# Performance work log

Hardware: AMD Instinct MI355X
Metric: run time of the kernel (lower is better)

The kernel has to match this reference:

```python
import jax, jax.numpy as jnp
import numpy as np

CURV_BOUNDS = (-2.0, 2.0)
THRESH = 0.01   # |k| below this -> Euclidean branch
EPS = 1e-5

B, S, D = 4, 2048, 512


def setup_inputs() -> dict:
    key = jax.random.key(0)
    ks = jax.random.split(key, 8)
    x = jax.random.normal(ks[0], (B, S, D), jnp.float32)
    sc = 1.0 / np.sqrt(D)  # ~ nn.Linear default init scale
    Wq = jax.random.uniform(ks[1], (D, D), jnp.float32, -sc, sc)
    bq = jax.random.uniform(ks[2], (D,), jnp.float32, -sc, sc)
    Wk = jax.random.uniform(ks[3], (D, D), jnp.float32, -sc, sc)
    bk = jax.random.uniform(ks[4], (D,), jnp.float32, -sc, sc)
    Wv = jax.random.uniform(ks[5], (D, D), jnp.float32, -sc, sc)
    bv = jax.random.uniform(ks[6], (D,), jnp.float32, -sc, sc)
    curvature_raw = jnp.float32(0.5)   # init_curvature
    temperature = jnp.float32(1.0)
    mask = jnp.triu(jnp.ones((S, S), dtype=bool), 1)  # causal: True = masked out
    return {"x": x, "Wq": Wq, "bq": bq, "Wk": Wk, "bk": bk, "Wv": Wv,
            "bv": bv, "curvature_raw": curvature_raw,
            "temperature": temperature, "mask": mask}


def _curvature(raw):
    k_min, k_max = CURV_BOUNDS
    return k_min + (k_max - k_min) * (jnp.tanh(raw) + 1.0) / 2.0


def _project(u, k):
    # project_to_manifold: identity (euclid), Poincare-ball clip (k<0), sphere renorm (k>0)
    n = jnp.sqrt(jnp.sum(u * u, axis=-1, keepdims=True) + 1e-12)
    absk = jnp.abs(k)
    sk = jnp.sqrt(jnp.maximum(absk, EPS))
    max_norm = (1.0 - 1e-3) / sk                      # ball radius 1/sqrt(|k|)
    u_hyp = u * jnp.minimum(1.0, max_norm / n)
    u_sph = u / (n * sk)                              # sphere radius 1/sqrt(k)
    return jnp.where(absk < THRESH, u, jnp.where(k < 0, u_hyp, u_sph))


def reference(x, Wq, bq, Wk, bk, Wv, bv, curvature_raw, temperature, mask):
    k = _curvature(curvature_raw)
    q = x @ Wq.T + bq
    kk = x @ Wk.T + bk
    v = x @ Wv.T + bv
    qm = _project(q, k)
    km = _project(kk, k)

    # pairwise quantities without materializing [B,S,S,D]
    dots = jnp.einsum('bid,bjd->bij', qm, km)         # [B,S,S]
    qn2 = jnp.sum(qm * qm, axis=-1)                   # [B,S]
    kn2 = jnp.sum(km * km, axis=-1)                   # [B,S]
    diff2 = jnp.maximum(qn2[:, :, None] + kn2[:, None, :] - 2.0 * dots, 0.0)

    absk = jnp.abs(k)
    sk = jnp.sqrt(jnp.maximum(absk, EPS))

    d_euc = jnp.sqrt(diff2 + 1e-12)
    # hyperbolic (Poincare ball, c=|k|): acosh(1 + 2c|x-y|^2 / ((1-c|x|^2)(1-c|y|^2))) / sqrt(c)
    denom = jnp.maximum((1.0 - absk * qn2)[:, :, None] * (1.0 - absk * kn2)[:, None, :], EPS)
    arg = 1.0 + 2.0 * absk * diff2 / denom
    d_hyp = jnp.arccosh(jnp.maximum(arg, 1.0 + 1e-7)) / sk
    # spherical (radius 1/sqrt(k)): arccos(k * <x,y>) / sqrt(k)
    cosang = jnp.clip(absk * dots, -1.0 + 1e-7, 1.0 - 1e-7)
    d_sph = jnp.arccos(cosang) / sk

    dist = jnp.where(absk < THRESH, d_euc, jnp.where(k < 0, d_hyp, d_sph))

    scores = -dist / (temperature + 1e-8)
    scores = jnp.where(mask[None, :, :], -jnp.inf, scores)
    attention = jax.nn.softmax(scores, axis=-1)       # [B,S,S]
    output = jnp.einsum('bij,bjd->bid', attention, v) # [B,S,D]
    return output, attention
```

## Files before the change

### kernel.cpp

```cpp
#include <hip/hip_runtime.h>
#include <hip/hip_bf16.h>
#include <math.h>

typedef unsigned short u16;
typedef float float4e __attribute__((ext_vector_type(4)));
typedef short short8 __attribute__((ext_vector_type(8)));

#define SEQ 2048
#define DIM 512
#define NB  4

__device__ __forceinline__ float bf2f(u16 h) {
    return __uint_as_float(((unsigned)h) << 16);
}
__device__ __forceinline__ u16 f2bf(float f) {
    __hip_bfloat16 h = __float2bfloat16(f);
    return *reinterpret_cast<u16*>(&h);
}
__device__ __forceinline__ float curv_of(float raw) {
    return -2.0f + 2.0f * (tanhf(raw) + 1.0f);
}
__device__ __forceinline__ void gl_lds16(const u16* g, u16* lds) {
    __builtin_amdgcn_global_load_lds(
        (const __attribute__((address_space(1))) unsigned int*)g,
        (__attribute__((address_space(3))) unsigned int*)lds, 16, 0, 0);
}

__global__ __launch_bounds__(256) void cvt_all_kernel(
    const float* __restrict__ x, const float* __restrict__ Wq,
    const float* __restrict__ Wk, const float* __restrict__ Wv,
    u16* __restrict__ x_bf, u16* __restrict__ Wcat, float* __restrict__ lsum)
{
    int i = blockIdx.x * 256 + threadIdx.x;
    const int n_x = NB * SEQ * DIM, n_w = DIM * DIM;
    if (i < NB * SEQ) lsum[i] = 0.f;
    if (i < n_x) {
        x_bf[i] = f2bf(x[i]);
    } else if (i < n_x + 3 * n_w) {
        int j = i - n_x;
        const float* W = (j < n_w) ? Wq : (j < 2 * n_w ? Wk : Wv);
        int off = j % n_w;
        Wcat[j] = f2bf(W[off]);
    }
}

__global__ __launch_bounds__(256) void qkv_gemm_kernel(
    const u16* __restrict__ A,
    const u16* __restrict__ Bt,
    u16* __restrict__ C,
    const float* __restrict__ bq, const float* __restrict__ bk, const float* __restrict__ bv)
{
    int bn = blockIdx.x, bm = blockIdx.y;
    __shared__ __align__(16) u16 As[128 * 32];
    __shared__ __align__(16) u16 Bs[128 * 32];

    int t = threadIdx.x, wave = t >> 6, lane = t & 63;
    int wm = wave >> 1, wn = wave & 1;
    int lrow = lane & 15, quad = lane >> 4;
    int lr4 = lane >> 2, lch = lane & 3;

    float4e acc[4][4];
#pragma unroll
    for (int i = 0; i < 4; i++)
#pragma unroll
        for (int j = 0; j < 4; j++) acc[i][j] = (float4e){0.f, 0.f, 0.f, 0.f};

    for (int kt = 0; kt < 16; ++kt) {
        int k0 = kt << 5;
        __syncthreads();
#pragma unroll
        for (int h = 0; h < 2; ++h) {
            int q = wave + h * 4;
            int row = q * 16 + lr4;
            gl_lds16(A  + (size_t)(bm * 128 + row) * 512 + k0 + lch * 8, &As[q * 512]);
            gl_lds16(Bt + (size_t)(bn * 128 + row) * 512 + k0 + lch * 8, &Bs[q * 512]);
        }
        __syncthreads();

        short8 af[4], bfr[4];
#pragma unroll
        for (int im = 0; im < 4; im++)
            af[im] = *(const short8*)&As[(wm * 64 + im * 16 + lrow) * 32 + quad * 8];
#pragma unroll
        for (int in = 0; in < 4; in++)
            bfr[in] = *(const short8*)&Bs[(wn * 64 + in * 16 + lrow) * 32 + quad * 8];
#pragma unroll
        for (int im = 0; im < 4; im++)
#pragma unroll
            for (int in = 0; in < 4; in++)
                acc[im][in] = __builtin_amdgcn_mfma_f32_16x16x32_bf16(af[im], bfr[in], acc[im][in], 0, 0, 0);
    }

#pragma unroll
    for (int im = 0; im < 4; im++)
#pragma unroll
        for (int in = 0; in < 4; in++)
#pragma unroll
            for (int r = 0; r < 4; r++) {
                int i = bm * 128 + wm * 64 + im * 16 + quad * 4 + r;
                int j = bn * 128 + wn * 64 + in * 16 + lrow;
                float bias = (j < 512) ? bq[j] : (j < 1024 ? bk[j - 512] : bv[j - 1024]);
                C[(size_t)i * 1536 + j] = f2bf(acc[im][in][r] + bias);
            }
}

__global__ __launch_bounds__(256) void project_kernel(
    const u16* __restrict__ qkvh,
    u16* __restrict__ qm, u16* __restrict__ km,
    float* __restrict__ qn2, float* __restrict__ kn2,
    const float* __restrict__ curvp)
{
    int r = blockIdx.x;
    int t = threadIdx.x;
    float kv = curv_of(curvp[0]);
    float absk = fabsf(kv);
    float sk = sqrtf(fmaxf(absk, 1e-5f));

    const u16* qrow = qkvh + (size_t)r * 1536;
    const u16* krow = qrow + 512;
    float q0 = bf2f(qrow[t]), q1 = bf2f(qrow[t + 256]);
    float k0 = bf2f(krow[t]), k1 = bf2f(krow[t + 256]);

    float sq = q0 * q0 + q1 * q1;
    float s2 = k0 * k0 + k1 * k1;
#pragma unroll
    for (int off = 32; off > 0; off >>= 1) {
        sq += __shfl_down(sq, off);
        s2 += __shfl_down(s2, off);
    }
    __shared__ float rq[4], rk[4];
    int wave = t >> 6, lane = t & 63;
    if (lane == 0) { rq[wave] = sq; rk[wave] = s2; }
    __syncthreads();
    float n2q = rq[0] + rq[1] + rq[2] + rq[3];
    float n2k = rk[0] + rk[1] + rk[2] + rk[3];

    float sclq, sclk;
    {
        float nq = sqrtf(n2q + 1e-12f);
        float nk = sqrtf(n2k + 1e-12f);
        if (absk < 0.01f) { sclq = 1.f; sclk = 1.f; }
        else if (kv < 0.f) {
            float mx = (1.0f - 1e-3f) / sk;
            sclq = fminf(1.f, mx / nq);
            sclk = fminf(1.f, mx / nk);
        } else {
            sclq = 1.f / (nq * sk);
            sclk = 1.f / (nk * sk);
        }
    }
    if (t == 0) {
        qn2[r] = n2q * sclq * sclq;
        kn2[r] = n2k * sclk * sclk;
    }
    u16* qo = qm + (size_t)r * 512;
    u16* ko = km + (size_t)r * 512;
    qo[t]       = f2bf(q0 * sclq);
    qo[t + 256] = f2bf(q1 * sclq);
    ko[t]       = f2bf(k0 * sclk);
    ko[t + 256] = f2bf(k1 * sclk);
}

__global__ __launch_bounds__(256) void transpose_v_kernel(
    const u16* __restrict__ qkvh, u16* __restrict__ vT)
{
    __shared__ u16 tile[32][33];
    int b = blockIdx.z;
    int s0 = blockIdx.x * 32, d0 = blockIdx.y * 32;
    int tx = threadIdx.x, ty = threadIdx.y;
#pragma unroll
    for (int r = 0; r < 4; r++) {
        int s = s0 + ty + r * 8;
        tile[ty + r * 8][tx] = qkvh[(size_t)(b * SEQ + s) * 1536 + 1024 + d0 + tx];
    }
    __syncthreads();
#pragma unroll
    for (int r = 0; r < 4; r++) {
        int d = d0 + ty + r * 8;
        int s = s0 + tx;
        vT[((size_t)b * DIM + d) * SEQ + s] = tile[tx][ty + r * 8];
    }
}

__global__ __launch_bounds__(256) void scores_kernel(
    const u16* __restrict__ qm, const u16* __restrict__ km,
    const float* __restrict__ qn2v, const float* __restrict__ kn2v,
    float* __restrict__ attnF, u16* __restrict__ attnH, float* __restrict__ lsum,
    const float* __restrict__ curvp, const float* __restrict__ tempp)
{
    int bn = blockIdx.x, bm = blockIdx.y, b = blockIdx.z;
    if (bn > bm) return;

    __shared__ __align__(16) u16 As[64 * 32];
    __shared__ __align__(16) u16 Bs[64 * 32];

    int t = threadIdx.x, wave = t >> 6, lane = t & 63;
    int wr = wave >> 1, wc = wave & 1;
    int lrow = lane & 15, quad = lane >> 4;
    int lr4 = lane >> 2, lch = lane & 3;

    const u16* Ab = qm + (size_t)b * SEQ * DIM;
    const u16* Bb = km + (size_t)b * SEQ * DIM;

    float4e acc[2][2];
#pragma unroll
    for (int i = 0; i < 2; i++)
#pragma unroll
        for (int j = 0; j < 2; j++) acc[i][j] = (float4e){0.f, 0.f, 0.f, 0.f};

    for (int kt = 0; kt < 16; ++kt) {
        int k0 = kt << 5;
        __syncthreads();
        int row = wave * 16 + lr4;
        gl_lds16(Ab + (size_t)(bm * 64 + row) * 512 + k0 + lch * 8, &As[wave * 512]);
        gl_lds16(Bb + (size_t)(bn * 64 + row) * 512 + k0 + lch * 8, &Bs[wave * 512]);
        __syncthreads();

        short8 af[2], bfr[2];
#pragma unroll
        for (int im = 0; im < 2; im++)
            af[im] = *(const short8*)&As[(wr * 32 + im * 16 + lrow) * 32 + quad * 8];
#pragma unroll
        for (int in = 0; in < 2; in++)
            bfr[in] = *(const short8*)&Bs[(wc * 32 + in * 16 + lrow) * 32 + quad * 8];
#pragma unroll
        for (int im = 0; im < 2; im++)
#pragma unroll
            for (int in = 0; in < 2; in++)
                acc[im][in] = __builtin_amdgcn_mfma_f32_16x16x32_bf16(af[im], bfr[in], acc[im][in], 0, 0, 0);
    }

    float kv = curv_of(curvp[0]);
    float absk = fabsf(kv);
    float sk = sqrtf(fmaxf(absk, 1e-5f));
    float invT = 1.0f / (tempp[0] + 1e-8f);

    float* attF = attnF + (size_t)b * SEQ * SEQ;
    u16*   attH = attnH + (size_t)b * SEQ * SEQ;

    float psum[2][4];
#pragma unroll
    for (int im = 0; im < 2; im++)
#pragma unroll
        for (int r = 0; r < 4; r++) psum[im][r] = 0.f;

#pragma unroll
    for (int im = 0; im < 2; im++) {
#pragma unroll
        for (int r = 0; r < 4; r++) {
            int gi = bm * 64 + wr * 32 + im * 16 + quad * 4 + r;
            float qn = qn2v[b * SEQ + gi];
#pragma unroll
            for (int in = 0; in < 2; in++) {
                int gj = bn * 64 + wc * 32 + in * 16 + lrow;
                float kn = kn2v[b * SEQ + gj];
                float dot = acc[im][in][r];
                float diff2 = fmaxf(qn + kn - 2.f * dot, 0.f);
                float dist;
                if (absk < 0.01f) {
                    dist = sqrtf(diff2 + 1e-12f);
                } else if (kv < 0.f) {
                    float denom = fmaxf((1.f - absk * qn) * (1.f - absk * kn), 1e-5f);
                    float arg = fmaxf(1.f + 2.f * absk * diff2 / denom, 1.f + 1e-7f);
                    dist = acoshf(arg) / sk;
                } else {
                    float c = fminf(fmaxf(absk * dot, -1.f + 1e-7f), 1.f - 1e-7f);
                    dist = acosf(c) / sk;
                }
                float s = -dist * invT;
                float e = (gj <= gi) ? __expf(s) : 0.f;
                attF[(size_t)gi * SEQ + gj] = e;
                attH[(size_t)gi * SEQ + gj] = f2bf(e);
                psum[im][r] += e;
            }
        }
    }

#pragma unroll
    for (int im = 0; im < 2; im++)
#pragma unroll
        for (int r = 0; r < 4; r++) {
            float v = psum[im][r];
            v += __shfl_xor(v, 1);
            v += __shfl_xor(v, 2);
            v += __shfl_xor(v, 4);
            v += __shfl_xor(v, 8);
            if (lrow == 0) {
                int gi = bm * 64 + wr * 32 + im * 16 + quad * 4 + r;
                atomicAdd(&lsum[b * SEQ + gi], v);
            }
        }
}

__global__ __launch_bounds__(256) void pv_kernel(
    const u16* __restrict__ attnH,
    const u16* __restrict__ vT,
    const float* __restrict__ lsum,
    float* __restrict__ out)
{
    int bn = blockIdx.x, bm = blockIdx.y, b = blockIdx.z;

    __shared__ __align__(16) u16 As[64 * 32];
    __shared__ __align__(16) u16 Bs[64 * 32];

    int t = threadIdx.x, wave = t >> 6, lane = t & 63;
    int wr = wave >> 1, wc = wave & 1;
    int lrow = lane & 15, quad = lane >> 4;
    int lr4 = lane >> 2, lch = lane & 3;

    const u16* Ab = attnH + (size_t)b * SEQ * SEQ;
    const u16* Bb = vT + (size_t)b * DIM * SEQ;

    float4e acc[2][2];
#pragma unroll
    for (int i = 0; i < 2; i++)
#pragma unroll
        for (int j = 0; j < 2; j++) acc[i][j] = (float4e){0.f, 0.f, 0.f, 0.f};

    int kIters = (bm + 1) * 2;
    for (int kt = 0; kt < kIters; ++kt) {
        int k0 = kt << 5;
        __syncthreads();
        int row = wave * 16 + lr4;
        gl_lds16(Ab + (size_t)(bm * 64 + row) * SEQ + k0 + lch * 8, &As[wave * 512]);
        gl_lds16(Bb + (size_t)(bn * 64 + row) * SEQ + k0 + lch * 8, &Bs[wave * 512]);
        __syncthreads();

        short8 af[2], bfr[2];
#pragma unroll
        for (int im = 0; im < 2; im++)
            af[im] = *(const short8*)&As[(wr * 32 + im * 16 + lrow) * 32 + quad * 8];
#pragma unroll
        for (int in = 0; in < 2; in++)
            bfr[in] = *(const short8*)&Bs[(wc * 32 + in * 16 + lrow) * 32 + quad * 8];
#pragma unroll
        for (int im = 0; im < 2; im++)
#pragma unroll
            for (int in = 0; in < 2; in++)
                acc[im][in] = __builtin_amdgcn_mfma_f32_16x16x32_bf16(af[im], bfr[in], acc[im][in], 0, 0, 0);
    }

#pragma unroll
    for (int im = 0; im < 2; im++)
#pragma unroll
        for (int r = 0; r < 4; r++) {
            int gi = bm * 64 + wr * 32 + im * 16 + quad * 4 + r;
            float invl = 1.0f / lsum[b * SEQ + gi];
#pragma unroll
            for (int in = 0; in < 2; in++) {
                int gd = bn * 64 + wc * 32 + in * 16 + lrow;
                out[((size_t)b * SEQ + gi) * DIM + gd] = acc[im][in][r] * invl;
            }
        }
}

__global__ __launch_bounds__(256) void norm_attn_kernel(
    float* __restrict__ attnF, const float* __restrict__ lsum)
{
    int i = blockIdx.x, b = blockIdx.y, t = threadIdx.x;
    float inv = 1.0f / lsum[b * SEQ + i];
    float4* row = (float4*)(attnF + ((size_t)b * SEQ + i) * SEQ);
#pragma unroll
    for (int c = t; c < SEQ / 4; c += 256) {
        int j0 = c * 4;
        float4 v = row[c];
        v.x = (j0     <= i) ? v.x * inv : 0.f;
        v.y = (j0 + 1 <= i) ? v.y * inv : 0.f;
        v.z = (j0 + 2 <= i) ? v.z * inv : 0.f;
        v.w = (j0 + 3 <= i) ? v.w * inv : 0.f;
        row[c] = v;
    }
}

extern "C" void kernel_launch(void* const* d_in, const int* in_sizes, int n_in,
                              void* d_out, int out_size, void* d_ws, size_t ws_size,
                              hipStream_t stream) {
    (void)in_sizes; (void)n_in; (void)out_size; (void)ws_size;

    const float* x    = (const float*)d_in[0];
    const float* Wq   = (const float*)d_in[1];
    const float* bq   = (const float*)d_in[2];
    const float* Wk   = (const float*)d_in[3];
    const float* bk   = (const float*)d_in[4];
    const float* Wv   = (const float*)d_in[5];
    const float* bv   = (const float*)d_in[6];
    const float* curv = (const float*)d_in[7];
    const float* temp = (const float*)d_in[8];

    float* out   = (float*)d_out;
    float* attnF = out + (size_t)NB * SEQ * DIM;

    char* ws = (char*)d_ws;
    u16*   x_bf  = (u16*)(ws + 0);
    u16*   Wcat  = (u16*)(ws + 8388608);
    u16*   qkvh  = (u16*)(ws + 9961472);
    u16*   qm    = (u16*)(ws + 35127296);
    u16*   km    = (u16*)(ws + 43515904);
    u16*   vT    = (u16*)(ws + 51904512);
    float* qn2   = (float*)(ws + 60293120);
    float* kn2   = (float*)(ws + 60325888);
    float* lsum  = (float*)(ws + 60358656);
    u16*   attnH = (u16*)(ws + 0);

    {
        int n_tot = NB * SEQ * DIM + 3 * DIM * DIM;
        cvt_all_kernel<<<(n_tot + 255) / 256, 256, 0, stream>>>(x, Wq, Wk, Wv, x_bf, Wcat, lsum);
    }

    {
        dim3 g(1536 / 128, 8192 / 128, 1);
        qkv_gemm_kernel<<<g, 256, 0, stream>>>(x_bf, Wcat, qkvh, bq, bk, bv);
    }

    project_kernel<<<NB * SEQ, 256, 0, stream>>>(qkvh, qm, km, qn2, kn2, curv);

    {
        dim3 g(SEQ / 32, DIM / 32, NB), blk(32, 8);
        transpose_v_kernel<<<g, blk, 0, stream>>>(qkvh, vT);
    }

    {
        dim3 g(SEQ / 64, SEQ / 64, NB);
        scores_kernel<<<g, 256, 0, stream>>>(qm, km, qn2, kn2, attnF, attnH, lsum, curv, temp);
    }

    {
        dim3 g(DIM / 64, SEQ / 64, NB);
        pv_kernel<<<g, 256, 0, stream>>>(attnH, vT, lsum, out);
    }

    norm_attn_kernel<<<dim3(SEQ, NB), 256, 0, stream>>>(attnF, lsum);
}
```

Baseline: 265.9 us.

## Unify GEMMs into templated 64x64 kernel with deeper K tiles and swizzled LDS

```diff
diff --git a/kernel.cpp b/kernel.cpp
--- a/kernel.cpp
+++ b/kernel.cpp
@@ -5,6 +5,7 @@
 typedef unsigned short u16;
 typedef float float4e __attribute__((ext_vector_type(4)));
 typedef short short8 __attribute__((ext_vector_type(8)));
+typedef unsigned short ushort8 __attribute__((ext_vector_type(8)));
 
 #define SEQ 2048
 #define DIM 512
@@ -44,64 +45,167 @@
     }
 }
 
-__global__ __launch_bounds__(256) void qkv_gemm_kernel(
-    const u16* __restrict__ A,
-    const u16* __restrict__ Bt,
-    u16* __restrict__ C,
-    const float* __restrict__ bq, const float* __restrict__ bk, const float* __restrict__ bv)
-{
-    int bn = blockIdx.x, bm = blockIdx.y;
-    __shared__ __align__(16) u16 As[128 * 32];
-    __shared__ __align__(16) u16 Bs[128 * 32];
-
+template<int MODE>
+__global__ __launch_bounds__(256) void gemm64_kernel(
+    const u16* __restrict__ A, int lda, long long sA,
+    const u16* __restrict__ Bt, int ldb, long long sB,
+    void* __restrict__ Cv, int ldc, long long sC,
+    float* __restrict__ lsum,
+    const float* __restrict__ bq, const float* __restrict__ bk, const float* __restrict__ bv,
+    const float* __restrict__ qn2v, const float* __restrict__ kn2v,
+    const float* __restrict__ curvp, const float* __restrict__ tempp)
+{
+    int bn = blockIdx.x, bm = blockIdx.y, b = blockIdx.z;
     int t = threadIdx.x, wave = t >> 6, lane = t & 63;
-    int wm = wave >> 1, wn = wave & 1;
+
+    if (MODE == 1) {
+        if (bn > bm) {
+            if (bn == bm + 1 && !(bm & 1)) {
+                u16* Cb = (u16*)Cv + (size_t)b * sC;
+                int r = t >> 2, seg = t & 3;
+                int4 z = {0, 0, 0, 0};
+                int4* p = (int4*)&Cb[(size_t)(bm * 64 + r) * ldc + bn * 64 + seg * 16];
+                p[0] = z; p[1] = z;
+            }
+            return;
+        }
+    }
+
+    __shared__ __align__(16) u16 As[64 * 128];
+    __shared__ __align__(16) u16 Bs[64 * 128];
+
+    int wr = wave >> 1, wc = wave & 1;
     int lrow = lane & 15, quad = lane >> 4;
-    int lr4 = lane >> 2, lch = lane & 3;
-
-    float4e acc[4][4];
-#pragma unroll
-    for (int i = 0; i < 4; i++)
-#pragma unroll
-        for (int j = 0; j < 4; j++) acc[i][j] = (float4e){0.f, 0.f, 0.f, 0.f};
-
-    for (int kt = 0; kt < 16; ++kt) {
-        int k0 = kt << 5;
+    int rl = lane >> 4, cs = lane & 15;
+
+    const u16* Ab = A + (size_t)b * sA + (size_t)(bm * 64) * lda;
+    const u16* Bb = Bt + (size_t)b * sB + (size_t)(bn * 64) * ldb;
+
+    float4e acc[2][2];
+#pragma unroll
+    for (int i = 0; i < 2; i++)
+#pragma unroll
+        for (int j = 0; j < 2; j++) acc[i][j] = (float4e){0.f, 0.f, 0.f, 0.f};
+
+    int kIters = (MODE == 2) ? ((bm + 2) >> 1) : 4;
+
+    for (int kt = 0; kt < kIters; ++kt) {
+        int k0 = kt << 7;
         __syncthreads();
 #pragma unroll
-        for (int h = 0; h < 2; ++h) {
-            int q = wave + h * 4;
-            int row = q * 16 + lr4;
-            gl_lds16(A  + (size_t)(bm * 128 + row) * 512 + k0 + lch * 8, &As[q * 512]);
-            gl_lds16(Bt + (size_t)(bn * 128 + row) * 512 + k0 + lch * 8, &Bs[q * 512]);
+        for (int h = 0; h < 4; ++h) {
+            int row = wave * 16 + h * 4 + rl;
+            int c = cs ^ (row & 15);
+            gl_lds16(Ab + (size_t)row * lda + k0 + c * 8, &As[(wave * 16 + h * 4) * 128]);
+            gl_lds16(Bb + (size_t)row * ldb + k0 + c * 8, &Bs[(wave * 16 + h * 4) * 128]);
         }
         __syncthreads();
-
-        short8 af[4], bfr[4];
-#pragma unroll
-        for (int im = 0; im < 4; im++)
-            af[im] = *(const short8*)&As[(wm * 64 + im * 16 + lrow) * 32 + quad * 8];
-#pragma unroll
-        for (int in = 0; in < 4; in++)
-            bfr[in] = *(const short8*)&Bs[(wn * 64 + in * 16 + lrow) * 32 + quad * 8];
-#pragma unroll
-        for (int im = 0; im < 4; im++)
-#pragma unroll
-            for (int in = 0; in < 4; in++)
-                acc[im][in] = __builtin_amdgcn_mfma_f32_16x16x32_bf16(af[im], bfr[in], acc[im][in], 0, 0, 0);
-    }
-
-#pragma unroll
-    for (int im = 0; im < 4; im++)
-#pragma unroll
-        for (int in = 0; in < 4; in++)
+#pragma unroll
+        for (int s = 0; s < 4; ++s) {
+            short8 af[2], bfr[2];
+#pragma unroll
+            for (int im = 0; im < 2; im++) {
+                int row = wr * 32 + im * 16 + lrow;
+                af[im] = *(const short8*)&As[(row * 16 + ((s * 4 + quad) ^ (row & 15))) * 8];
+            }
+#pragma unroll
+            for (int in = 0; in < 2; in++) {
+                int row = wc * 32 + in * 16 + lrow;
+                bfr[in] = *(const short8*)&Bs[(row * 16 + ((s * 4 + quad) ^ (row & 15))) * 8];
+            }
+#pragma unroll
+            for (int im = 0; im < 2; im++)
+#pragma unroll
+                for (int in = 0; in < 2; in++)
+                    acc[im][in] = __builtin_amdgcn_mfma_f32_16x16x32_bf16(af[im], bfr[in], acc[im][in], 0, 0, 0);
+        }
+    }
+
+    if (MODE == 0) {
+        u16* Cb = (u16*)Cv;
+#pragma unroll
+        for (int im = 0; im < 2; im++)
+#pragma unroll
+            for (int in = 0; in < 2; in++)
+#pragma unroll
+                for (int r = 0; r < 4; r++) {
+                    int gi = bm * 64 + wr * 32 + im * 16 + quad * 4 + r;
+                    int gj = bn * 64 + wc * 32 + in * 16 + lrow;
+                    float bias = (gj < 512) ? bq[gj] : (gj < 1024 ? bk[gj - 512] : bv[gj - 1024]);
+                    Cb[(size_t)gi * ldc + gj] = f2bf(acc[im][in][r] + bias);
+                }
+    } else if (MODE == 1) {
+        float kv = curv_of(curvp[0]);
+        float absk = fabsf(kv);
+        float sk = sqrtf(fmaxf(absk, 1e-5f));
+        float invT = 1.0f / (tempp[0] + 1e-8f);
+        u16* Cb = (u16*)Cv + (size_t)b * sC;
+
+        float psum[2][4];
+#pragma unroll
+        for (int im = 0; im < 2; im++)
+#pragma unroll
+            for (int r = 0; r < 4; r++) psum[im][r] = 0.f;
+
+#pragma unroll
+        for (int im = 0; im < 2; im++) {
 #pragma unroll
             for (int r = 0; r < 4; r++) {
-                int i = bm * 128 + wm * 64 + im * 16 + quad * 4 + r;
-                int j = bn * 128 + wn * 64 + in * 16 + lrow;
-                float bias = (j < 512) ? bq[j] : (j < 1024 ? bk[j - 512] : bv[j - 1024]);
-                C[(size_t)i * 1536 + j] = f2bf(acc[im][in][r] + bias);
-            }
+                int gi = bm * 64 + wr * 32 + im * 16 + quad * 4 + r;
+                float qn = qn2v[b * SEQ + gi];
+#pragma unroll
+                for (int in = 0; in < 2; in++) {
+                    int gj = bn * 64 + wc * 32 + in * 16 + lrow;
+                    float kn = kn2v[b * SEQ + gj];
+                    float dot = acc[im][in][r];
+                    float diff2 = fmaxf(qn + kn - 2.f * dot, 0.f);
+                    float dist;
+                    if (absk < 0.01f) {
+                        dist = sqrtf(diff2 + 1e-12f);
+                    } else if (kv < 0.f) {
+                        float denom = fmaxf((1.f - absk * qn) * (1.f - absk * kn), 1e-5f);
+                        float arg = fmaxf(1.f + 2.f * absk * diff2 / denom, 1.f + 1e-7f);
+                        dist = acoshf(arg) / sk;
+                    } else {
+                        float c = fminf(fmaxf(absk * dot, -1.f + 1e-7f), 1.f - 1e-7f);
+                        dist = acosf(c) / sk;
+                    }
+                    float s = -dist * invT;
+                    float e = (gj <= gi) ? __expf(s) : 0.f;
+                    Cb[(size_t)gi * ldc + gj] = f2bf(e);
+                    psum[im][r] += e;
+                }
+            }
+        }
+#pragma unroll
+        for (int im = 0; im < 2; im++)
+#pragma unroll
+            for (int r = 0; r < 4; r++) {
+                float v = psum[im][r];
+                v += __shfl_xor(v, 1);
+                v += __shfl_xor(v, 2);
+                v += __shfl_xor(v, 4);
+                v += __shfl_xor(v, 8);
+                if (lrow == 0) {
+                    int gi = bm * 64 + wr * 32 + im * 16 + quad * 4 + r;
+                    atomicAdd(&lsum[b * SEQ + gi], v);
+                }
+            }
+    } else {
+        float* Cb = (float*)Cv + (size_t)b * sC;
+#pragma unroll
+        for (int im = 0; im < 2; im++)
+#pragma unroll
+            for (int r = 0; r < 4; r++) {
+                int gi = bm * 64 + wr * 32 + im * 16 + quad * 4 + r;
+                float invl = 1.0f / lsum[b * SEQ + gi];
+#pragma unroll
+                for (int in = 0; in < 2; in++) {
+                    int gd = bn * 64 + wc * 32 + in * 16 + lrow;
+                    Cb[(size_t)gi * ldc + gd] = acc[im][in][r] * invl;
+                }
+            }
+    }
 }
 
 __global__ __launch_bounds__(256) void project_kernel(
@@ -182,194 +286,33 @@
     }
 }
 
-__global__ __launch_bounds__(256) void scores_kernel(
-    const u16* __restrict__ qm, const u16* __restrict__ km,
-    const float* __restrict__ qn2v, const float* __restrict__ kn2v,
-    float* __restrict__ attnF, u16* __restrict__ attnH, float* __restrict__ lsum,
-    const float* __restrict__ curvp, const float* __restrict__ tempp)
-{
-    int bn = blockIdx.x, bm = blockIdx.y, b = blockIdx.z;
-    if (bn > bm) return;
-
-    __shared__ __align__(16) u16 As[64 * 32];
-    __shared__ __align__(16) u16 Bs[64 * 32];
-
-    int t = threadIdx.x, wave = t >> 6, lane = t & 63;
-    int wr = wave >> 1, wc = wave & 1;
-    int lrow = lane & 15, quad = lane >> 4;
-    int lr4 = lane >> 2, lch = lane & 3;
-
-    const u16* Ab = qm + (size_t)b * SEQ * DIM;
-    const u16* Bb = km + (size_t)b * SEQ * DIM;
-
-    float4e acc[2][2];
-#pragma unroll
-    for (int i = 0; i < 2; i++)
-#pragma unroll
-        for (int j = 0; j < 2; j++) acc[i][j] = (float4e){0.f, 0.f, 0.f, 0.f};
-
-    for (int kt = 0; kt < 16; ++kt) {
-        int k0 = kt << 5;
-        __syncthreads();
-        int row = wave * 16 + lr4;
-        gl_lds16(Ab + (size_t)(bm * 64 + row) * 512 + k0 + lch * 8, &As[wave * 512]);
-        gl_lds16(Bb + (size_t)(bn * 64 + row) * 512 + k0 + lch * 8, &Bs[wave * 512]);
-        __syncthreads();
-
-        short8 af[2], bfr[2];
-#pragma unroll
-        for (int im = 0; im < 2; im++)
-            af[im] = *(const short8*)&As[(wr * 32 + im * 16 + lrow) * 32 + quad * 8];
-#pragma unroll
-        for (int in = 0; in < 2; in++)
-            bfr[in] = *(const short8*)&Bs[(wc * 32 + in * 16 + lrow) * 32 + quad * 8];
-#pragma unroll
-        for (int im = 0; im < 2; im++)
-#pragma unroll
-            for (int in = 0; in < 2; in++)
-                acc[im][in] = __builtin_amdgcn_mfma_f32_16x16x32_bf16(af[im], bfr[in], acc[im][in], 0, 0, 0);
-    }
-
-    float kv = curv_of(curvp[0]);
-    float absk = fabsf(kv);
-    float sk = sqrtf(fmaxf(absk, 1e-5f));
-    float invT = 1.0f / (tempp[0] + 1e-8f);
-
-    float* attF = attnF + (size_t)b * SEQ * SEQ;
-    u16*   attH = attnH + (size_t)b * SEQ * SEQ;
-
-    float psum[2][4];
-#pragma unroll
-    for (int im = 0; im < 2; im++)
-#pragma unroll
-        for (int r = 0; r < 4; r++) psum[im][r] = 0.f;
-
-#pragma unroll
-    for (int im = 0; im < 2; im++) {
-#pragma unroll
-        for (int r = 0; r < 4; r++) {
-            int gi = bm * 64 + wr * 32 + im * 16 + quad * 4 + r;
-            float qn = qn2v[b * SEQ + gi];
-#pragma unroll
-            for (int in = 0; in < 2; in++) {
-                int gj = bn * 64 + wc * 32 + in * 16 + lrow;
-                float kn = kn2v[b * SEQ + gj];
-                float dot = acc[im][in][r];
-                float diff2 = fmaxf(qn + kn - 2.f * dot, 0.f);
-                float dist;
-                if (absk < 0.01f) {
-                    dist = sqrtf(diff2 + 1e-12f);
-                } else if (kv < 0.f) {
-                    float denom = fmaxf((1.f - absk * qn) * (1.f - absk * kn), 1e-5f);
-                    float arg = fmaxf(1.f + 2.f * absk * diff2 / denom, 1.f + 1e-7f);
-                    dist = acoshf(arg) / sk;
-                } else {
-                    float c = fminf(fmaxf(absk * dot, -1.f + 1e-7f), 1.f - 1e-7f);
-                    dist = acosf(c) / sk;
-                }
-                float s = -dist * invT;
-                float e = (gj <= gi) ? __expf(s) : 0.f;
-                attF[(size_t)gi * SEQ + gj] = e;
-                attH[(size_t)gi * SEQ + gj] = f2bf(e);
-                psum[im][r] += e;
-            }
-        }
-    }
-
-#pragma unroll
-    for (int im = 0; im < 2; im++)
-#pragma unroll
-        for (int r = 0; r < 4; r++) {
-            float v = psum[im][r];
-            v += __shfl_xor(v, 1);
-            v += __shfl_xor(v, 2);
-            v += __shfl_xor(v, 4);
-            v += __shfl_xor(v, 8);
-            if (lrow == 0) {
-                int gi = bm * 64 + wr * 32 + im * 16 + quad * 4 + r;
-                atomicAdd(&lsum[b * SEQ + gi], v);
-            }
-        }
-}
-
-__global__ __launch_bounds__(256) void pv_kernel(
-    const u16* __restrict__ attnH,
-    const u16* __restrict__ vT,
-    const float* __restrict__ lsum,
-    float* __restrict__ out)
-{
-    int bn = blockIdx.x, bm = blockIdx.y, b = blockIdx.z;
-
-    __shared__ __align__(16) u16 As[64 * 32];
-    __shared__ __align__(16) u16 Bs[64 * 32];
-
-    int t = threadIdx.x, wave = t >> 6, lane = t & 63;
-    int wr = wave >> 1, wc = wave & 1;
-    int lrow = lane & 15, quad = lane >> 4;
-    int lr4 = lane >> 2, lch = lane & 3;
-
-    const u16* Ab = attnH + (size_t)b * SEQ * SEQ;
-    const u16* Bb = vT + (size_t)b * DIM * SEQ;
-
-    float4e acc[2][2];
-#pragma unroll
-    for (int i = 0; i < 2; i++)
-#pragma unroll
-        for (int j = 0; j < 2; j++) acc[i][j] = (float4e){0.f, 0.f, 0.f, 0.f};
-
-    int kIters = (bm + 1) * 2;
-    for (int kt = 0; kt < kIters; ++kt) {
-        int k0 = kt << 5;
-        __syncthreads();
-        int row = wave * 16 + lr4;
-        gl_lds16(Ab + (size_t)(bm * 64 + row) * SEQ + k0 + lch * 8, &As[wave * 512]);
-        gl_lds16(Bb + (size_t)(bn * 64 + row) * SEQ + k0 + lch * 8, &Bs[wave * 512]);
-        __syncthreads();
-
-        short8 af[2], bfr[2];
-#pragma unroll
-        for (int im = 0; im < 2; im++)
-            af[im] = *(const short8*)&As[(wr * 32 + im * 16 + lrow) * 32 + quad * 8];
-#pragma unroll
-        for (int in = 0; in < 2; in++)
-            bfr[in] = *(const short8*)&Bs[(wc * 32 + in * 16 + lrow) * 32 + quad * 8];
-#pragma unroll
-        for (int im = 0; im < 2; im++)
-#pragma unroll
-            for (int in = 0; in < 2; in++)
-                acc[im][in] = __builtin_amdgcn_mfma_f32_16x16x32_bf16(af[im], bfr[in], acc[im][in], 0, 0, 0);
-    }
-
-#pragma unroll
-    for (int im = 0; im < 2; im++)
-#pragma unroll
-        for (int r = 0; r < 4; r++) {
-            int gi = bm * 64 + wr * 32 + im * 16 + quad * 4 + r;
-            float invl = 1.0f / lsum[b * SEQ + gi];
-#pragma unroll
-            for (int in = 0; in < 2; in++) {
-                int gd = bn * 64 + wc * 32 + in * 16 + lrow;
-                out[((size_t)b * SEQ + gi) * DIM + gd] = acc[im][in][r] * invl;
-            }
-        }
-}
-
 __global__ __launch_bounds__(256) void norm_attn_kernel(
-    float* __restrict__ attnF, const float* __restrict__ lsum)
+    const u16* __restrict__ attnH, const float* __restrict__ lsum,
+    float* __restrict__ attnF)
 {
     int i = blockIdx.x, b = blockIdx.y, t = threadIdx.x;
     float inv = 1.0f / lsum[b * SEQ + i];
-    float4* row = (float4*)(attnF + ((size_t)b * SEQ + i) * SEQ);
-#pragma unroll
-    for (int c = t; c < SEQ / 4; c += 256) {
-        int j0 = c * 4;
-        float4 v = row[c];
-        v.x = (j0     <= i) ? v.x * inv : 0.f;
-        v.y = (j0 + 1 <= i) ? v.y * inv : 0.f;
-        v.z = (j0 + 2 <= i) ? v.z * inv : 0.f;
-        v.w = (j0 + 3 <= i) ? v.w * inv : 0.f;
-        row[c] = v;
-    }
+    const u16* rowh = attnH + ((size_t)b * SEQ + i) * SEQ;
+    float* row = attnF + ((size_t)b * SEQ + i) * SEQ;
+    int L = i + 1;
+    int j0 = t * 8;
+    float4 lo, hi;
+    if (j0 + 8 <= L) {
+        ushort8 h = *(const ushort8*)&rowh[j0];
+        lo.x = bf2f(h[0]) * inv; lo.y = bf2f(h[1]) * inv;
+        lo.z = bf2f(h[2]) * inv; lo.w = bf2f(h[3]) * inv;
+        hi.x = bf2f(h[4]) * inv; hi.y = bf2f(h[5]) * inv;
+        hi.z = bf2f(h[6]) * inv; hi.w = bf2f(h[7]) * inv;
+    } else {
+        float v[8];
+#pragma unroll
+        for (int e = 0; e < 8; e++)
+            v[e] = (j0 + e < L) ? bf2f(rowh[j0 + e]) * inv : 0.f;
+        lo = (float4){v[0], v[1], v[2], v[3]};
+        hi = (float4){v[4], v[5], v[6], v[7]};
+    }
+    *(float4*)&row[j0] = lo;
+    *(float4*)&row[j0 + 4] = hi;
 }
 
 extern "C" void kernel_launch(void* const* d_in, const int* in_sizes, int n_in,
@@ -407,10 +350,9 @@
         cvt_all_kernel<<<(n_tot + 255) / 256, 256, 0, stream>>>(x, Wq, Wk, Wv, x_bf, Wcat, lsum);
     }
 
-    {
-        dim3 g(1536 / 128, 8192 / 128, 1);
-        qkv_gemm_kernel<<<g, 256, 0, stream>>>(x_bf, Wcat, qkvh, bq, bk, bv);
-    }
+    gemm64_kernel<0><<<dim3(1536 / 64, 8192 / 64, 1), 256, 0, stream>>>(
+        x_bf, 512, 0, Wcat, 512, 0, (void*)qkvh, 1536, 0,
+        nullptr, bq, bk, bv, nullptr, nullptr, nullptr, nullptr);
 
     project_kernel<<<NB * SEQ, 256, 0, stream>>>(qkvh, qm, km, qn2, kn2, curv);
 
@@ -419,15 +361,15 @@
         transpose_v_kernel<<<g, blk, 0, stream>>>(qkvh, vT);
     }
 
-    {
-        dim3 g(SEQ / 64, SEQ / 64, NB);
-        scores_kernel<<<g, 256, 0, stream>>>(qm, km, qn2, kn2, attnF, attnH, lsum, curv, temp);
-    }
-
-    {
-        dim3 g(DIM / 64, SEQ / 64, NB);
-        pv_kernel<<<g, 256, 0, stream>>>(attnH, vT, lsum, out);
-    }
-
-    norm_attn_kernel<<<dim3(SEQ, NB), 256, 0, stream>>>(attnF, lsum);
-}
+    gemm64_kernel<1><<<dim3(SEQ / 64, SEQ / 64, NB), 256, 0, stream>>>(
+        qm, 512, (long long)SEQ * DIM, km, 512, (long long)SEQ * DIM,
+        (void*)attnH, SEQ, (long long)SEQ * SEQ,
+        lsum, nullptr, nullptr, nullptr, qn2, kn2, curv, temp);
+
+    gemm64_kernel<2><<<dim3(DIM / 64, SEQ / 64, NB), 256, 0, stream>>>(
+        attnH, SEQ, (long long)SEQ * SEQ, vT, SEQ, (long long)DIM * SEQ,
+        (void*)out, DIM, (long long)SEQ * DIM,
+        lsum, nullptr, nullptr, nullptr, nullptr, nullptr, nullptr, nullptr);
+
+    norm_attn_kernel<<<dim3(SEQ, NB), 256, 0, stream>>>(attnH, lsum, attnF);
+}
```

Result: faster. 251.0 us (-5.6%).
